# Kernel optimization log

Measured on AMD Instinct MI355X. Metric: run time of the kernel, lower is better.

Reference implementation:

```python
import jax, jax.numpy as jnp
import numpy as np

SEG = 256  # segment_size from init_kwargs


def setup_inputs() -> dict:
    key = jax.random.key(0)
    ks = jax.random.split(key, 8)
    B, Lq, Lkv, D, H, dk = 2, 1024, 2048, 1024, 16, 64
    s = 1.0 / np.sqrt(D)
    return {
        "q": jax.random.normal(ks[0], (B, Lq, D), jnp.float32),
        "k": jax.random.normal(ks[1], (B, Lkv, D), jnp.float32),
        "v": jax.random.normal(ks[2], (B, Lkv, D), jnp.float32),
        "Wq": jax.random.normal(ks[3], (H, D, dk), jnp.float32) * s,
        "bq": jnp.zeros((H, dk), jnp.float32),
        "Wk": jax.random.normal(ks[4], (H, D, dk), jnp.float32) * s,
        "bk": jnp.zeros((H, dk), jnp.float32),
        "Wv": jax.random.normal(ks[5], (D, dk), jnp.float32) * s,
        "bv": jnp.zeros((dk,), jnp.float32),
        "Wh": jax.random.normal(ks[6], (dk, D), jnp.float32) * s,
    }


def reference(q, k, v, Wq, bq, Wk, bk, Wv, bv, Wh):
    B, Lq, D = q.shape
    kv_len = k.shape[1]
    S = SEG
    nseg = kv_len // S  # kv_len divisible by S -> no padding branch
    H, _, dk = Wq.shape
    dv = Wv.shape[-1]

    kseg = k.reshape(B, nseg, S, D)
    vseg = v.reshape(B, nseg, S, D)

    # per-head linear projections
    qs = jnp.einsum('bqd,hdk->bhqk', q, Wq) + bq[:, None, :]            # [B,H,Lq,dk]
    kp = jnp.einsum('bnsd,hdk->bhnsk', kseg, Wk) + bk[:, None, None, :]  # [B,H,n,S,dk]
    vp = jnp.einsum('bnsd,dv->bnsv', vseg, Wv) + bv                      # [B,n,S,dv]

    scale = jnp.sqrt(jnp.asarray(dk, q.dtype))
    attn = jnp.einsum('bhqk,bhnsk->bhnqs', qs, kp) / scale               # [B,H,n,Lq,S]
    # SAME causal mask applied to every segment (no offset), as in source
    causal = jnp.triu(jnp.ones((Lq, S), bool), k=1)
    attn = jnp.where(causal, jnp.asarray(-1e9, attn.dtype), attn)
    attn = jax.nn.softmax(attn, axis=-1)

    out = jnp.einsum('bhnqs,bnsv->bhnqv', attn, vp)                      # [B,H,n,Lq,dv]

    L = nseg * Lq  # segments concatenated along query dim (segment-major)
    head = out.reshape(B, H, L, dv).transpose(0, 2, 1, 3)                # [B,L,H,dv]
    attn_out = attn.reshape(B, H, L, S).transpose(0, 2, 1, 3)            # [B,L,H,S]

    outputs = head.mean(axis=2) @ Wh                                     # [B,L,D]
    return outputs, attn_out
```

## Files before the change

### kernel.cpp

```cpp
#include <hip/hip_runtime.h>


#define B_ 2
#define LQ 1024
#define LKV 2048
#define D_ 1024
#define H_ 16
#define DK 64
#define SEGW 256
#define NSEG 8
#define LTOT 8192

typedef _Float16 f16;
typedef __attribute__((ext_vector_type(8))) _Float16 f16x8;
typedef __attribute__((ext_vector_type(4))) _Float16 f16x4;
typedef __attribute__((ext_vector_type(4))) float f32x4;

#define MFMA_F16(a, b, c) __builtin_amdgcn_mfma_f32_16x16x32_f16((a), (b), (c), 0, 0, 0)

__global__ __launch_bounds__(256) void prep_kernel(
    const float* __restrict__ Wq, const float* __restrict__ Wk,
    const float* __restrict__ Wv, const float* __restrict__ Wh,
    f16* __restrict__ WqT, f16* __restrict__ WkT, f16* __restrict__ WvT,
    f16* __restrict__ WhT) {
  __shared__ float T[32][33];
  const int bid = blockIdx.x;
  const float* src;
  f16* dst;
  int D, N, d0, n0;
  size_t soff = 0, doff = 0;
  if (bid < 2048) {
    int z = bid >> 6, inner = bid & 63;
    int h = z & 15;
    src = (z < 16) ? Wq : Wk;
    dst = (z < 16) ? WqT : WkT;
    soff = (size_t)h * (1024 * 64);
    doff = (size_t)h * (64 * 1024);
    D = 1024; N = 64;
    d0 = (inner & 31) * 32;
    n0 = (inner >> 5) * 32;
  } else if (bid < 2112) {
    int i = bid - 2048;
    src = Wv; dst = WvT; D = 1024; N = 64;
    d0 = (i & 31) * 32;
    n0 = (i >> 5) * 32;
  } else {
    int i = bid - 2112;
    src = Wh; dst = WhT; D = 64; N = 1024;
    d0 = (i & 1) * 32;
    n0 = (i >> 1) * 32;
  }
  const int c = threadIdx.x & 31, r0 = threadIdx.x >> 5;
#pragma unroll
  for (int i = 0; i < 4; ++i) {
    int r = r0 + i * 8;
    T[r][c] = src[soff + (size_t)(d0 + r) * N + n0 + c];
  }
  __syncthreads();
#pragma unroll
  for (int i = 0; i < 4; ++i) {
    int rr = r0 + i * 8;
    dst[doff + (size_t)(n0 + rr) * D + d0 + c] = (f16)T[c][rr];
  }
}

__device__ __forceinline__ void proj_body(
    const float* __restrict__ A, const f16* __restrict__ WT,
    const float* __restrict__ bias, f16* __restrict__ C, int Mb, int bshift,
    int m0, int c0, char* smem) {
  f16(*Ah)[40] = (f16(*)[40])smem;
  f16(*Bh)[40] = (f16(*)[40])(smem + 10240);
  const int tid = threadIdx.x, lane = tid & 63, w = tid >> 6;
  const int wr = w >> 1, wc = w & 1;
  const int l15 = lane & 15, l4 = lane >> 4;

  f32x4 acc[4][4];
#pragma unroll
  for (int i = 0; i < 4; ++i)
#pragma unroll
    for (int j = 0; j < 4; ++j) acc[i][j] = (f32x4)0.f;

  for (int k0 = 0; k0 < 1024; k0 += 32) {
    __syncthreads();
    {
      int f4 = tid & 7, row0 = tid >> 3;
#pragma unroll
      for (int p = 0; p < 4; ++p) {
        int r = row0 + p * 32;
        float4 a = *(const float4*)(A + (size_t)(m0 + r) * 1024 + k0 + f4 * 4);
        f16x4 h4;
        h4[0] = (f16)a.x; h4[1] = (f16)a.y; h4[2] = (f16)a.z; h4[3] = (f16)a.w;
        *(f16x4*)&Ah[r][f4 * 4] = h4;
      }
      int u = tid & 3, cb = tid >> 2;
#pragma unroll
      for (int p = 0; p < 2; ++p) {
        int cc = cb + p * 64;
        *(f16x8*)&Bh[cc][u * 8] =
            *(const f16x8*)(WT + (size_t)(c0 + cc) * 1024 + k0 + u * 8);
      }
    }
    __syncthreads();
    f16x8 ah[4], bh[4];
#pragma unroll
    for (int i = 0; i < 4; ++i) {
      ah[i] = *(const f16x8*)&Ah[wr * 64 + i * 16 + l15][l4 * 8];
      bh[i] = *(const f16x8*)&Bh[wc * 64 + i * 16 + l15][l4 * 8];
    }
#pragma unroll
    for (int i = 0; i < 4; ++i)
#pragma unroll
      for (int j = 0; j < 4; ++j) acc[i][j] = MFMA_F16(ah[i], bh[j], acc[i][j]);
  }

#pragma unroll
  for (int j = 0; j < 4; ++j) {
    int c = c0 + wc * 64 + j * 16 + l15;
    float bs = bias[c];
    int hidx = c >> 6, dk = c & 63;
#pragma unroll
    for (int i = 0; i < 4; ++i) {
#pragma unroll
      for (int r = 0; r < 4; ++r) {
        int m = m0 + wr * 64 + i * 16 + l4 * 4 + r;
        int b = m >> bshift;
        int ml = m - (b << bshift);
        C[((size_t)(b * 16 + hidx) * Mb + ml) * 64 + dk] = (f16)(acc[i][j][r] + bs);
      }
    }
  }
}

__device__ __forceinline__ void vproj_body(
    const float* __restrict__ v, const f16* __restrict__ WvT,
    const float* __restrict__ bv, f16* __restrict__ vpTg, int m0, char* smem) {
  f16(*Av)[40] = (f16(*)[40])smem;
  f16(*Bv)[40] = (f16(*)[40])(smem + 5120);
  const int tid = threadIdx.x, lane = tid & 63, w = tid >> 6;
  const int l15 = lane & 15, l4 = lane >> 4;

  f32x4 acc[4];
#pragma unroll
  for (int j = 0; j < 4; ++j) acc[j] = (f32x4)0.f;

  for (int k0 = 0; k0 < 1024; k0 += 32) {
    __syncthreads();
    {
      int f4 = tid & 7, row0 = tid >> 3;
#pragma unroll
      for (int p = 0; p < 2; ++p) {
        int r = row0 + p * 32;
        float4 a = *(const float4*)(v + (size_t)(m0 + r) * 1024 + k0 + f4 * 4);
        f16x4 h4;
        h4[0] = (f16)a.x; h4[1] = (f16)a.y; h4[2] = (f16)a.z; h4[3] = (f16)a.w;
        *(f16x4*)&Av[r][f4 * 4] = h4;
      }
      int u = tid & 3, cb = tid >> 2;
      *(f16x8*)&Bv[cb][u * 8] =
          *(const f16x8*)(WvT + (size_t)cb * 1024 + k0 + u * 8);
    }
    __syncthreads();
    f16x8 a8 = *(const f16x8*)&Av[w * 16 + l15][l4 * 8];
#pragma unroll
    for (int cf = 0; cf < 4; ++cf) {
      f16x8 b8 = *(const f16x8*)&Bv[cf * 16 + l15][l4 * 8];
      acc[cf] = MFMA_F16(a8, b8, acc[cf]);
    }
  }
#pragma unroll
  for (int cf = 0; cf < 4; ++cf) {
    int dv = cf * 16 + l15;
    float bvv = bv[dv];
#pragma unroll
    for (int r = 0; r < 4; ++r) {
      int m = m0 + w * 16 + l4 * 4 + r;
      int b = m >> 11, rest = m & 2047, n = rest >> 8, si = rest & 255;
      vpTg[((size_t)((b * 8 + n) * 64 + dv)) * 256 + si] = (f16)(acc[cf][r] + bvv);
    }
  }
}

__global__ __launch_bounds__(256) void proj_all_kernel(
    const float* __restrict__ q, const float* __restrict__ k,
    const float* __restrict__ v, const f16* __restrict__ WqT,
    const f16* __restrict__ WkT, const f16* __restrict__ WvT,
    const float* __restrict__ bq, const float* __restrict__ bk,
    const float* __restrict__ bv, f16* __restrict__ qs, f16* __restrict__ kp,
    f16* __restrict__ vpTg) {
  __shared__ __align__(16) char smem[20480];
  const int bid = blockIdx.x;
  if (bid < 128) {
    proj_body(q, WqT, bq, qs, 1024, 10, (bid & 15) * 128, (bid >> 4) * 128, smem);
  } else if (bid < 384) {
    int i = bid - 128;
    proj_body(k, WkT, bk, kp, 2048, 11, (i & 31) * 128, (i >> 5) * 128, smem);
  } else {
    vproj_body(v, WvT, bv, vpTg, (bid - 384) * 64, smem);
  }
}

__global__ __launch_bounds__(256, 2) void fused_attn_kernel(
    const f16* __restrict__ qs, const f16* __restrict__ kp,
    const f16* __restrict__ vpTg, float* __restrict__ attn_out,
    f16* __restrict__ mhp) {
  __shared__ __align__(16) char Kbuf[2][32768];

  const int bid = blockIdx.x;
  const int xcd = bid & 7, sub = bid >> 3;
  const int gg = xcd * 4 + (sub >> 4);
  const int qt = sub & 15;
  const int pair = gg & 15, hgIdx = gg >> 4;
  const int b = pair >> 3, n = pair & 7;
  const int q0 = qt * 64;

  const int tid = threadIdx.x, lane = tid & 63, w = tid >> 6;
  const int l15 = lane & 15, l4 = lane >> 4;

  const int laneoff =
      (lane >> 3) * 128 + (((lane & 7) * 16) ^ ((lane >> 3) << 4));

  f16x8 vfrag[8];
  {
    const f16* vb = vpTg + ((size_t)(pair * 64 + w * 16 + l15)) * 256 + l4 * 8;
#pragma unroll
    for (int kc = 0; kc < 8; ++kc) vfrag[kc] = *(const f16x8*)(vb + kc * 32);
  }

#define STAGE_K(bufIdx, h)                                                      \
  {                                                                             \
    const char* src_ = (const char*)kp +                                        \
        ((size_t)((b * 16 + (h)) * 2048 + n * 256)) * 128;                      \
    char* lds_ = &Kbuf[bufIdx][0];                                              \
    _Pragma("unroll")                                                           \
    for (int j_ = 0; j_ < 8; ++j_) {                                            \
      int ch_ = w * 8 + j_;                                                     \
      __builtin_amdgcn_global_load_lds(                                         \
          (const __attribute__((address_space(1))) unsigned int*)(src_ +        \
              ch_ * 1024 + laneoff),                                            \
          (__attribute__((address_space(3))) unsigned int*)(lds_ + ch_ * 1024), \
          16, 0, 0);                                                            \
    }                                                                           \
  }

#define LOAD_Q(h, a0, a1)                                                       \
  {                                                                             \
    const f16* qp_ = qs +                                                       \
        ((size_t)((b * 16 + (h)) * 1024 + q0 + w * 16 + l15)) * 64 + l4 * 8;    \
    a0 = *(const f16x8*)qp_;                                                    \
    a1 = *(const f16x8*)(qp_ + 32);                                             \
  }

  f16x8 qa0, qa1, qn0, qn1;
  STAGE_K(0, hgIdx * 8);
  LOAD_Q(hgIdx * 8, qa0, qa1);
  qn0 = qa0; qn1 = qa1;

  f32x4 accO[4];
#pragma unroll
  for (int i = 0; i < 4; ++i) accO[i] = (f32x4)0.f;

  asm volatile("s_waitcnt vmcnt(2)" ::: "memory");
  __builtin_amdgcn_s_barrier();

#pragma unroll 1
  for (int hh = 0; hh < 8; ++hh) {
    const int h = hgIdx * 8 + hh;
    const int cur = hh & 1;
    if (hh < 7) {
      STAGE_K(cur ^ 1, h + 1);
      LOAD_Q(h + 1, qn0, qn1);
    }

    f32x4 accS[16];
#pragma unroll
    for (int sf = 0; sf < 16; ++sf) accS[sf] = (f32x4)0.f;
    const char* Kc = &Kbuf[cur][0];
    {
      const int sw = (l15 & 7) << 4;
      __builtin_amdgcn_s_setprio(1);
#pragma unroll
      for (int sf = 0; sf < 16; ++sf) {
        const int rowb = (sf * 16 + l15) * 128;
        f16x8 b0 = *(const f16x8*)(Kc + rowb + ((l4 * 16) ^ sw));
        f16x8 b1 = *(const f16x8*)(Kc + rowb + ((64 + l4 * 16) ^ sw));
        accS[sf] = MFMA_F16(qa0, b0, accS[sf]);
        accS[sf] = MFMA_F16(qa1, b1, accS[sf]);
      }
      __builtin_amdgcn_s_setprio(0);
    }

    float inv[4];
#pragma unroll
    for (int r = 0; r < 4; ++r) {
      const int qg = q0 + w * 16 + l4 * 4 + r;
      float mx = -3.0e38f;
#pragma unroll
      for (int sf = 0; sf < 16; ++sf) {
        int s = sf * 16 + l15;
        float vv = accS[sf][r] * 0.125f;
        if (s > qg) vv = -3.0e38f;
        accS[sf][r] = vv;
        mx = fmaxf(mx, vv);
      }
      mx = fmaxf(mx, __shfl_xor(mx, 1));
      mx = fmaxf(mx, __shfl_xor(mx, 2));
      mx = fmaxf(mx, __shfl_xor(mx, 4));
      mx = fmaxf(mx, __shfl_xor(mx, 8));
      float sum = 0.f;
#pragma unroll
      for (int sf = 0; sf < 16; ++sf) {
        float e = __expf(accS[sf][r] - mx);
        accS[sf][r] = e;
        sum += e;
      }
      sum += __shfl_xor(sum, 1);
      sum += __shfl_xor(sum, 2);
      sum += __shfl_xor(sum, 4);
      sum += __shfl_xor(sum, 8);
      inv[r] = 1.0f / sum;
    }

    asm volatile("s_waitcnt lgkmcnt(0)" ::: "memory");
    __builtin_amdgcn_s_barrier();

    char* Pc = &Kbuf[cur][0];
#pragma unroll
    for (int r = 0; r < 4; ++r) {
      const int q = w * 16 + l4 * 4 + r;
      const int sw = (q & 7) << 4;
      const int rowb = q * 512;
#pragma unroll
      for (int sf = 0; sf < 16; ++sf) {
        int s = sf * 16 + l15;
        *(f16*)(Pc + rowb + ((s * 2) ^ sw)) = (f16)(accS[sf][r] * inv[r]);
      }
    }
    asm volatile("s_waitcnt lgkmcnt(0)" ::: "memory");
    __builtin_amdgcn_s_barrier();

    {
      const size_t base0 =
          (((size_t)b * LTOT + (size_t)n * LQ + q0) * H_ + h) * SEGW;
#pragma unroll
      for (int it = 0; it < 16; ++it) {
        const int q = w * 16 + it;
        f16x4 p4 =
            *(const f16x4*)(Pc + q * 512 + ((lane * 8) ^ ((q & 7) << 4)));
        f32x4 f;
        f[0] = (float)p4[0]; f[1] = (float)p4[1];
        f[2] = (float)p4[2]; f[3] = (float)p4[3];
        __builtin_nontemporal_store(
            f, (f32x4*)(attn_out + base0 + (size_t)q * (H_ * SEGW) + lane * 4));
      }
    }

    __builtin_amdgcn_s_setprio(1);
#pragma unroll
    for (int kc = 0; kc < 8; ++kc) {
#pragma unroll
      for (int qb = 0; qb < 4; ++qb) {
        const int q = qb * 16 + l15;
        f16x8 pa = *(const f16x8*)(Pc + q * 512 +
                                   ((kc * 64 + l4 * 16) ^ ((q & 7) << 4)));
        accO[qb] = MFMA_F16(pa, vfrag[kc], accO[qb]);
      }
    }
    __builtin_amdgcn_s_setprio(0);

    qa0 = qn0; qa1 = qn1;
    asm volatile("s_waitcnt lgkmcnt(0)" ::: "memory");
    asm volatile("s_waitcnt vmcnt(16)" ::: "memory");
    __builtin_amdgcn_s_barrier();
  }

  {
    f16* mp = mhp + ((size_t)hgIdx * 16384 + (size_t)pair * 1024 + q0) * 64 +
              w * 16 + l15;
    const float s16 = 1.0f / 16.0f;
#pragma unroll
    for (int qb = 0; qb < 4; ++qb)
#pragma unroll
      for (int r = 0; r < 4; ++r)
        mp[(size_t)(qb * 16 + l4 * 4 + r) * 64] = (f16)(accO[qb][r] * s16);
  }
#undef STAGE_K
#undef LOAD_Q
}

__global__ __launch_bounds__(256) void final_f16_kernel(
    const f16* __restrict__ mhp, const f16* __restrict__ WhT,
    float* __restrict__ outputs) {
  __shared__ f16 Af[64][72], Bf[128][72];
  const int m0 = blockIdx.x * 64, c0 = blockIdx.y * 128;
  const int tid = threadIdx.x, lane = tid & 63, w = tid >> 6;
  const int l15 = lane & 15, l4 = lane >> 4;
  {
    int u = tid & 7, row0 = tid >> 3;
#pragma unroll
    for (int p = 0; p < 2; ++p) {
      int r = row0 + p * 32;
      size_t mi = (size_t)(m0 + r) * 64 + u * 8;
      f16x8 a0 = *(const f16x8*)(mhp + mi);
      f16x8 a1 = *(const f16x8*)(mhp + (size_t)16384 * 64 + mi);
      *(f16x8*)&Af[r][u * 8] = a0 + a1;
    }
    int cb = tid >> 3;
#pragma unroll
    for (int p = 0; p < 4; ++p) {
      int c = cb + p * 32;
      *(f16x8*)&Bf[c][u * 8] = *(const f16x8*)(WhT + (size_t)(c0 + c) * 64 + u * 8);
    }
  }
  __syncthreads();

  f32x4 acc[8];
#pragma unroll
  for (int cf = 0; cf < 8; ++cf) acc[cf] = (f32x4)0.f;
#pragma unroll
  for (int kc = 0; kc < 2; ++kc) {
    f16x8 a8 = *(const f16x8*)&Af[w * 16 + l15][kc * 32 + l4 * 8];
#pragma unroll
    for (int cf = 0; cf < 8; ++cf) {
      f16x8 b8 = *(const f16x8*)&Bf[cf * 16 + l15][kc * 32 + l4 * 8];
      acc[cf] = MFMA_F16(a8, b8, acc[cf]);
    }
  }
#pragma unroll
  for (int cf = 0; cf < 8; ++cf)
#pragma unroll
    for (int r = 0; r < 4; ++r)
      __builtin_nontemporal_store(
          acc[cf][r], outputs + (size_t)(m0 + w * 16 + l4 * 4 + r) * 1024 + c0 +
                          cf * 16 + l15);
}

extern "C" void kernel_launch(void* const* d_in, const int* in_sizes, int n_in,
                              void* d_out, int out_size, void* d_ws,
                              size_t ws_size, hipStream_t stream) {
  const float* q  = (const float*)d_in[0];
  const float* k  = (const float*)d_in[1];
  const float* v  = (const float*)d_in[2];
  const float* Wq = (const float*)d_in[3];
  const float* bq = (const float*)d_in[4];
  const float* Wk = (const float*)d_in[5];
  const float* bk = (const float*)d_in[6];
  const float* Wv = (const float*)d_in[7];
  const float* bv = (const float*)d_in[8];
  const float* Wh = (const float*)d_in[9];

  float* outputs  = (float*)d_out;
  float* attn_out = (float*)d_out + (size_t)B_ * LTOT * D_;

  char* ws = (char*)d_ws;
  f16* WqT  = (f16*)(ws + 0);
  f16* WkT  = (f16*)(ws + (2u << 20));
  f16* WvT  = (f16*)(ws + (4u << 20));
  f16* WhT  = (f16*)(ws + (4u << 20) + 131072);
  f16* qs   = (f16*)(ws + (4u << 20) + 262144);
  f16* kp   = (f16*)((char*)qs + (4u << 20));
  f16* vpTg = (f16*)((char*)kp + (8u << 20));
  f16* mhp  = (f16*)((char*)vpTg + (1u << 19));

  prep_kernel<<<dim3(2176), 256, 0, stream>>>(Wq, Wk, Wv, Wh, WqT, WkT, WvT, WhT);
  proj_all_kernel<<<dim3(448), 256, 0, stream>>>(q, k, v, WqT, WkT, WvT, bq, bk,
                                                 bv, qs, kp, vpTg);
  fused_attn_kernel<<<dim3(512), 256, 0, stream>>>(qs, kp, vpTg, attn_out, mhp);
  final_f16_kernel<<<dim3(256, 8), 256, 0, stream>>>(mhp, WhT, outputs);
}
```

Measured before the change: 131.1 us.

## Double-buffer projection GEMM tiles with register prefetch and reorder PV before attn store

The projection GEMMs (q/k per-head and v) now prefetch the next k-slice into registers while MFMAs run on the current LDS buffer, using two LDS buffers and one barrier per iteration instead of two. Shared memory doubles to 40 KB, which may reduce occupancy of the projection kernel. In the attention kernel, the P·V MFMA block is moved ahead of the attn_out streaming stores so compute is issued before the large global writes.

```diff
diff --git a/kernel.cpp b/kernel.cpp
--- a/kernel.cpp
+++ b/kernel.cpp
@@ -69,10 +69,12 @@
     const float* __restrict__ bias, f16* __restrict__ C, int Mb, int bshift,
     int m0, int c0, char* smem) {
   f16(*Ah)[40] = (f16(*)[40])smem;
-  f16(*Bh)[40] = (f16(*)[40])(smem + 10240);
+  f16(*Bh)[40] = (f16(*)[40])(smem + 20480);
   const int tid = threadIdx.x, lane = tid & 63, w = tid >> 6;
   const int wr = w >> 1, wc = w & 1;
   const int l15 = lane & 15, l4 = lane >> 4;
+  const int f4 = tid & 7, row0 = tid >> 3;
+  const int u = tid & 3, cb = tid >> 2;
 
   f32x4 acc[4][4];
 #pragma unroll
@@ -80,38 +82,53 @@
 #pragma unroll
     for (int j = 0; j < 4; ++j) acc[i][j] = (f32x4)0.f;
 
-  for (int k0 = 0; k0 < 1024; k0 += 32) {
+  float4 aR[4];
+  f16x8 bR[2];
+
+#define PLOAD(k0)                                                              \
+  {                                                                            \
+    _Pragma("unroll") for (int p = 0; p < 4; ++p) aR[p] =                      \
+        *(const float4*)(A + (size_t)(m0 + row0 + p * 32) * 1024 + (k0) +      \
+                         f4 * 4);                                              \
+    _Pragma("unroll") for (int p = 0; p < 2; ++p) bR[p] =                      \
+        *(const f16x8*)(WT + (size_t)(c0 + cb + p * 64) * 1024 + (k0) +        \
+                        u * 8);                                                \
+  }
+#define PSTORE(bi)                                                             \
+  {                                                                            \
+    _Pragma("unroll") for (int p = 0; p < 4; ++p) {                            \
+      f16x4 h4;                                                                \
+      h4[0] = (f16)aR[p].x; h4[1] = (f16)aR[p].y;                              \
+      h4[2] = (f16)aR[p].z; h4[3] = (f16)aR[p].w;                              \
+      *(f16x4*)&Ah[(bi)*128 + row0 + p * 32][f4 * 4] = h4;                     \
+    }                                                                          \
+    _Pragma("unroll") for (int p = 0; p < 2; ++p)                              \
+        *(f16x8*)&Bh[(bi)*128 + cb + p * 64][u * 8] = bR[p];                   \
+  }
+
+  PLOAD(0);
+  PSTORE(0);
+  __syncthreads();
+
+#pragma unroll 2
+  for (int k = 0; k < 32; ++k) {
+    if (k + 1 < 32) PLOAD((k + 1) * 32);
+    const int cbuf = (k & 1) * 128;
+    f16x8 ah[4], bh[4];
+#pragma unroll
+    for (int i = 0; i < 4; ++i) {
+      ah[i] = *(const f16x8*)&Ah[cbuf + wr * 64 + i * 16 + l15][l4 * 8];
+      bh[i] = *(const f16x8*)&Bh[cbuf + wc * 64 + i * 16 + l15][l4 * 8];
+    }
+#pragma unroll
+    for (int i = 0; i < 4; ++i)
+#pragma unroll
+      for (int j = 0; j < 4; ++j) acc[i][j] = MFMA_F16(ah[i], bh[j], acc[i][j]);
+    if (k + 1 < 32) PSTORE((k + 1) & 1);
     __syncthreads();
-    {
-      int f4 = tid & 7, row0 = tid >> 3;
-#pragma unroll
-      for (int p = 0; p < 4; ++p) {
-        int r = row0 + p * 32;
-        float4 a = *(const float4*)(A + (size_t)(m0 + r) * 1024 + k0 + f4 * 4);
-        f16x4 h4;
-        h4[0] = (f16)a.x; h4[1] = (f16)a.y; h4[2] = (f16)a.z; h4[3] = (f16)a.w;
-        *(f16x4*)&Ah[r][f4 * 4] = h4;
-      }
-      int u = tid & 3, cb = tid >> 2;
-#pragma unroll
-      for (int p = 0; p < 2; ++p) {
-        int cc = cb + p * 64;
-        *(f16x8*)&Bh[cc][u * 8] =
-            *(const f16x8*)(WT + (size_t)(c0 + cc) * 1024 + k0 + u * 8);
-      }
-    }
-    __syncthreads();
-    f16x8 ah[4], bh[4];
-#pragma unroll
-    for (int i = 0; i < 4; ++i) {
-      ah[i] = *(const f16x8*)&Ah[wr * 64 + i * 16 + l15][l4 * 8];
-      bh[i] = *(const f16x8*)&Bh[wc * 64 + i * 16 + l15][l4 * 8];
-    }
-#pragma unroll
-    for (int i = 0; i < 4; ++i)
-#pragma unroll
-      for (int j = 0; j < 4; ++j) acc[i][j] = MFMA_F16(ah[i], bh[j], acc[i][j]);
-  }
+  }
+#undef PLOAD
+#undef PSTORE
 
 #pragma unroll
   for (int j = 0; j < 4; ++j) {
@@ -135,38 +152,57 @@
     const float* __restrict__ v, const f16* __restrict__ WvT,
     const float* __restrict__ bv, f16* __restrict__ vpTg, int m0, char* smem) {
   f16(*Av)[40] = (f16(*)[40])smem;
-  f16(*Bv)[40] = (f16(*)[40])(smem + 5120);
+  f16(*Bv)[40] = (f16(*)[40])(smem + 10240);
   const int tid = threadIdx.x, lane = tid & 63, w = tid >> 6;
   const int l15 = lane & 15, l4 = lane >> 4;
+  const int f4 = tid & 7, row0 = tid >> 3;
+  const int u = tid & 3, cb = tid >> 2;
 
   f32x4 acc[4];
 #pragma unroll
   for (int j = 0; j < 4; ++j) acc[j] = (f32x4)0.f;
 
-  for (int k0 = 0; k0 < 1024; k0 += 32) {
+  float4 aR[2];
+  f16x8 bR;
+
+#define VLOAD(k0)                                                              \
+  {                                                                            \
+    _Pragma("unroll") for (int p = 0; p < 2; ++p) aR[p] =                      \
+        *(const float4*)(v + (size_t)(m0 + row0 + p * 32) * 1024 + (k0) +      \
+                         f4 * 4);                                              \
+    bR = *(const f16x8*)(WvT + (size_t)cb * 1024 + (k0) + u * 8);              \
+  }
+#define VSTORE(bi)                                                             \
+  {                                                                            \
+    _Pragma("unroll") for (int p = 0; p < 2; ++p) {                            \
+      f16x4 h4;                                                                \
+      h4[0] = (f16)aR[p].x; h4[1] = (f16)aR[p].y;                              \
+      h4[2] = (f16)aR[p].z; h4[3] = (f16)aR[p].w;                              \
+      *(f16x4*)&Av[(bi)*64 + row0 + p * 32][f4 * 4] = h4;                      \
+    }                                                                          \
+    *(f16x8*)&Bv[(bi)*64 + cb][u * 8] = bR;                                    \
+  }
+
+  VLOAD(0);
+  VSTORE(0);
+  __syncthreads();
+
+#pragma unroll 2
+  for (int k = 0; k < 32; ++k) {
+    if (k + 1 < 32) VLOAD((k + 1) * 32);
+    const int cbuf = (k & 1) * 64;
+    f16x8 a8 = *(const f16x8*)&Av[cbuf + w * 16 + l15][l4 * 8];
+#pragma unroll
+    for (int cf = 0; cf < 4; ++cf) {
+      f16x8 b8 = *(const f16x8*)&Bv[cbuf + cf * 16 + l15][l4 * 8];
+      acc[cf] = MFMA_F16(a8, b8, acc[cf]);
+    }
+    if (k + 1 < 32) VSTORE((k + 1) & 1);
     __syncthreads();
-    {
-      int f4 = tid & 7, row0 = tid >> 3;
-#pragma unroll
-      for (int p = 0; p < 2; ++p) {
-        int r = row0 + p * 32;
-        float4 a = *(const float4*)(v + (size_t)(m0 + r) * 1024 + k0 + f4 * 4);
-        f16x4 h4;
-        h4[0] = (f16)a.x; h4[1] = (f16)a.y; h4[2] = (f16)a.z; h4[3] = (f16)a.w;
-        *(f16x4*)&Av[r][f4 * 4] = h4;
-      }
-      int u = tid & 3, cb = tid >> 2;
-      *(f16x8*)&Bv[cb][u * 8] =
-          *(const f16x8*)(WvT + (size_t)cb * 1024 + k0 + u * 8);
-    }
-    __syncthreads();
-    f16x8 a8 = *(const f16x8*)&Av[w * 16 + l15][l4 * 8];
-#pragma unroll
-    for (int cf = 0; cf < 4; ++cf) {
-      f16x8 b8 = *(const f16x8*)&Bv[cf * 16 + l15][l4 * 8];
-      acc[cf] = MFMA_F16(a8, b8, acc[cf]);
-    }
-  }
+  }
+#undef VLOAD
+#undef VSTORE
+
 #pragma unroll
   for (int cf = 0; cf < 4; ++cf) {
     int dv = cf * 16 + l15;
@@ -187,7 +223,7 @@
     const float* __restrict__ bq, const float* __restrict__ bk,
     const float* __restrict__ bv, f16* __restrict__ qs, f16* __restrict__ kp,
     f16* __restrict__ vpTg) {
-  __shared__ __align__(16) char smem[20480];
+  __shared__ __align__(16) char smem[40960];
   const int bid = blockIdx.x;
   if (bid < 128) {
     proj_body(q, WqT, bq, qs, 1024, 10, (bid & 15) * 128, (bid >> 4) * 128, smem);
@@ -338,6 +374,19 @@
     asm volatile("s_waitcnt lgkmcnt(0)" ::: "memory");
     __builtin_amdgcn_s_barrier();
 
+    __builtin_amdgcn_s_setprio(1);
+#pragma unroll
+    for (int kc = 0; kc < 8; ++kc) {
+#pragma unroll
+      for (int qb = 0; qb < 4; ++qb) {
+        const int q = qb * 16 + l15;
+        f16x8 pa = *(const f16x8*)(Pc + q * 512 +
+                                   ((kc * 64 + l4 * 16) ^ ((q & 7) << 4)));
+        accO[qb] = MFMA_F16(pa, vfrag[kc], accO[qb]);
+      }
+    }
+    __builtin_amdgcn_s_setprio(0);
+
     {
       const size_t base0 =
           (((size_t)b * LTOT + (size_t)n * LQ + q0) * H_ + h) * SEGW;
@@ -353,19 +402,6 @@
             f, (f32x4*)(attn_out + base0 + (size_t)q * (H_ * SEGW) + lane * 4));
       }
     }
-
-    __builtin_amdgcn_s_setprio(1);
-#pragma unroll
-    for (int kc = 0; kc < 8; ++kc) {
-#pragma unroll
-      for (int qb = 0; qb < 4; ++qb) {
-        const int q = qb * 16 + l15;
-        f16x8 pa = *(const f16x8*)(Pc + q * 512 +
-                                   ((kc * 64 + l4 * 16) ^ ((q & 7) << 4)));
-        accO[qb] = MFMA_F16(pa, vfrag[kc], accO[qb]);
-      }
-    }
-    __builtin_amdgcn_s_setprio(0);
 
     qa0 = qn0; qa1 = qn1;
     asm volatile("s_waitcnt lgkmcnt(0)" ::: "memory");
```

New measurement: 125.5 us. 4.3% less time.
